# Kernel optimization log

Hardware: AMD Instinct MI355X
Metric: run time of the kernel (lower is better)

The kernel has to match this reference:

```python
import jax, jax.numpy as jnp
import numpy as np

TOP_K = 2


def setup_inputs() -> dict:
    key = jax.random.key(0)
    ks = jax.random.split(key, 7)
    B, T, C, E = 4, 2048, 1024, 8
    H = 4 * C
    s = 0.02
    return {
        "x": jax.random.normal(ks[0], (B, T, C), dtype=jnp.float32),
        "w_gate": jax.random.normal(ks[1], (C, E), dtype=jnp.float32) * s,
        "w1": jax.random.normal(ks[2], (E, C, H), dtype=jnp.float32) * s,
        "b1": jnp.zeros((E, H), dtype=jnp.float32),
        "w2": jax.random.normal(ks[3], (E, H, C), dtype=jnp.float32) * s,
        "b2": jnp.zeros((E, C), dtype=jnp.float32),
    }


def reference(x, w_gate, w1, b1, w2, b2):
    # Eval-mode MoE: noiseless gating (self.training=False), dropout inactive.
    B, T, C = x.shape
    E = w1.shape[0]
    xf = x.reshape(-1, C)                                # [N, C]
    logits = xf @ w_gate                                 # [N, E] clean logits
    top_vals, top_idx = jax.lax.top_k(logits, TOP_K)     # [N, K]
    scores = jax.nn.softmax(top_vals, axis=-1)           # [N, K]
    out = jnp.zeros_like(xf)
    for e in range(E):                                   # fixed small expert loop
        # combine weight per token for expert e (0 if not routed -> same math
        # as the original masked gather/scatter, since 0*expert_out == 0)
        w = jnp.sum(scores * (top_idx == e), axis=-1)    # [N]
        h = jax.nn.gelu(xf @ w1[e] + b1[e], approximate=False)  # [N, 4C]
        y = h @ w2[e] + b2[e]                            # [N, C]
        out = out + w[:, None] * y
    return out.reshape(B, T, C)
```

## Files before the change

kernel.cpp:

```cpp
#include <hip/hip_runtime.h>

#define NTOK 8192
#define CDIM 1024
#define ENUM 8
#define HDIM 4096

typedef unsigned short u16;
typedef unsigned int u32;
typedef __attribute__((ext_vector_type(8))) short s16x8;
typedef __attribute__((ext_vector_type(4))) float f32x4;
typedef __attribute__((ext_vector_type(4))) u32 u32x4;
typedef __attribute__((ext_vector_type(2))) u32 u32x2;

static __device__ __forceinline__ u16 f2bf(float f) {
  union { float f; u32 u; } v; v.f = f;
  u32 r = v.u + 0x7fffu + ((v.u >> 16) & 1u);
  return (u16)(r >> 16);
}
static __device__ __forceinline__ u32 pack2(float a, float b) {
  return (u32)f2bf(a) | ((u32)f2bf(b) << 16);
}
static __device__ __forceinline__ float bflo(u32 v) {
  union { u32 u; float f; } x; x.u = v << 16; return x.f;
}
static __device__ __forceinline__ float bfhi(u32 v) {
  union { u32 u; float f; } x; x.u = v & 0xffff0000u; return x.f;
}

typedef __attribute__((address_space(1))) const void gvoid;
typedef __attribute__((address_space(3))) void lvoid;
static __device__ __forceinline__ void gload16(const u16* g, u16* l) {
  __builtin_amdgcn_global_load_lds((gvoid*)g, (lvoid*)l, 16, 0, 0);
}

static __device__ __forceinline__ float gelu_fast(float v) {
  float u = v * (1.5957691216f + 0.1426929792f * v * v);
  return v / (1.f + __expf(-u));
}

__global__ void wconv_kernel(const float* __restrict__ w, u16* __restrict__ wt,
                             int K, int N) {
  __shared__ float lt[64][65];
  const int e = blockIdx.z, k0 = blockIdx.y * 64, n0 = blockIdx.x * 64;
  const float* src = w + (size_t)e * K * N;
  u16* dst = wt + (size_t)e * N * K;
  const int t = threadIdx.x;
  const int tr = t >> 4, tc = (t & 15) * 4;
#pragma unroll
  for (int i = 0; i < 4; ++i) {
    f32x4 v = __builtin_nontemporal_load(
        (const f32x4*)(src + (size_t)(k0 + tr + i * 16) * N + n0 + tc));
    lt[tr + i * 16][tc] = v.x; lt[tr + i * 16][tc + 1] = v.y;
    lt[tr + i * 16][tc + 2] = v.z; lt[tr + i * 16][tc + 3] = v.w;
  }
  __syncthreads();
#pragma unroll
  for (int i = 0; i < 4; ++i) {
    int n = tr + i * 16;
    uint2 o;
    o.x = pack2(lt[tc + 0][n], lt[tc + 1][n]);
    o.y = pack2(lt[tc + 2][n], lt[tc + 3][n]);
    *(uint2*)(dst + (size_t)(n0 + n) * K + k0 + tc) = o;
  }
}

__global__ void gate_kernel(const float* __restrict__ x, const float* __restrict__ wg,
                            int* __restrict__ cnt, int* __restrict__ tok_e,
                            float* __restrict__ tok_w) {
  __shared__ int lcnt[ENUM];
  const int tid = threadIdx.x;
  if (tid < ENUM) lcnt[tid] = 0;
  __syncthreads();
  const int wv = tid >> 6, lane = tid & 63;
  const int tbase = blockIdx.x * 32 + wv * 8;
  for (int t = 0; t < 8; ++t) {
    const int gw = tbase + t;
    const float* xr = x + (size_t)gw * CDIM;
    float acc[ENUM];
#pragma unroll
    for (int e = 0; e < ENUM; ++e) acc[e] = 0.f;
#pragma unroll 4
    for (int i = 0; i < CDIM / 64; ++i) {
      int c = i * 64 + lane;
      float xv = xr[c];
      float4 wa = *(const float4*)(wg + (size_t)c * ENUM);
      float4 wb = *(const float4*)(wg + (size_t)c * ENUM + 4);
      acc[0] += xv * wa.x; acc[1] += xv * wa.y; acc[2] += xv * wa.z; acc[3] += xv * wa.w;
      acc[4] += xv * wb.x; acc[5] += xv * wb.y; acc[6] += xv * wb.z; acc[7] += xv * wb.w;
    }
#pragma unroll
    for (int e = 0; e < ENUM; ++e) {
#pragma unroll
      for (int off = 32; off > 0; off >>= 1) acc[e] += __shfl_xor(acc[e], off);
    }
    if (lane == 0) {
      int i0 = 0; float v0 = acc[0];
#pragma unroll
      for (int e = 1; e < ENUM; ++e) if (acc[e] > v0) { v0 = acc[e]; i0 = e; }
      int i1 = -1; float v1 = -3.4e38f;
#pragma unroll
      for (int e = 0; e < ENUM; ++e) if (e != i0 && acc[e] > v1) { v1 = acc[e]; i1 = e; }
      float ex = expf(v1 - v0);
      float den = 1.f + ex;
      tok_e[gw * 2] = i0;     tok_w[gw * 2] = 1.f / den;
      tok_e[gw * 2 + 1] = i1; tok_w[gw * 2 + 1] = ex / den;
      atomicAdd(&lcnt[i0], 1); atomicAdd(&lcnt[i1], 1);
    }
  }
  __syncthreads();
  if (tid < ENUM) {
    int v = lcnt[tid];
    if (v) atomicAdd(&cnt[tid], v);
  }
}

__global__ void offsets_kernel(const int* __restrict__ cnt, int* __restrict__ offs) {
  if (threadIdx.x == 0 && blockIdx.x == 0) {
    int s = 0;
    for (int e = 0; e < ENUM; ++e) { offs[e] = s; s += cnt[e]; }
  }
}

__global__ void assign_kernel(const int* __restrict__ tok_e, const int* __restrict__ offs,
                              int* __restrict__ fill, int* __restrict__ slot_tok,
                              int* __restrict__ tok_slot) {
  __shared__ int lfill[ENUM], lbase[ENUM];
  const int tid = threadIdx.x;
  if (tid < ENUM) lfill[tid] = 0;
  __syncthreads();
  const int n = blockIdx.x * 256 + tid;
  const int e0 = tok_e[n * 2], e1 = tok_e[n * 2 + 1];
  const int p0 = atomicAdd(&lfill[e0], 1);
  const int p1 = atomicAdd(&lfill[e1], 1);
  __syncthreads();
  if (tid < ENUM) lbase[tid] = lfill[tid] ? atomicAdd(&fill[tid], lfill[tid]) : 0;
  __syncthreads();
  const int s0 = offs[e0] + lbase[e0] + p0;
  const int s1 = offs[e1] + lbase[e1] + p1;
  slot_tok[s0] = n; tok_slot[n * 2] = s0;
  slot_tok[s1] = n; tok_slot[n * 2 + 1] = s1;
}

__global__ void gather_kernel(const float* __restrict__ x, const int* __restrict__ slot_tok,
                              u16* __restrict__ xg) {
  int gid = blockIdx.x * blockDim.x + threadIdx.x;
  int slot = gid >> 8;
  int c4 = (gid & 255) * 4;
  int tok = slot_tok[slot];
  float4 v = *(const float4*)(x + (size_t)tok * CDIM + c4);
  uint2 o; o.x = pack2(v.x, v.y); o.y = pack2(v.z, v.w);
  *(uint2*)(xg + (size_t)slot * CDIM + c4) = o;
}

template <int PHASE>
__global__ __launch_bounds__(256, 2) void moe_gemm(
    const u16* __restrict__ Ag, const u16* __restrict__ Bt, const float* __restrict__ bias,
    u16* __restrict__ outp,
    const int* __restrict__ cnts, const int* __restrict__ offs,
    int K, int Nn) {
  const int e = blockIdx.z;
  const int cnt = cnts[e];
  const int NT = gridDim.x;
  const int MTC = gridDim.y >> 3;
  const int r = blockIdx.y * NT + blockIdx.x;
  const int k = r & 7;
  const int i = r >> 3;
  const int ck = (k + e) & 7;
  const int mt = ck * MTC + (i % MTC);
  const int nt = i / MTC;
  if (mt * 128 >= cnt) return;
  const int moff = offs[e];
  const int tid = threadIdx.x;
  const int wv = tid >> 6, ln = tid & 63;
  const int lr = ln & 15, lg = ln >> 4;
  const int wm = wv >> 1, wn = wv & 1;

  __shared__ __align__(16) u16 lds[2][128 * 64];
  u16* lA = lds[0];
  u16* lB = lds[1];

  const u16* Abase = Ag + (size_t)moff * K;
  const u16* Bbase = Bt + (size_t)e * Nn * K + (size_t)nt * 128 * K;

  const int srow = ln >> 3;
  const int sk = (((ln & 7) ^ srow)) * 8;

  f32x4 acc[4][4];
#pragma unroll
  for (int m = 0; m < 4; ++m)
#pragma unroll
    for (int n = 0; n < 4; ++n) {
      acc[m][n][0] = 0.f; acc[m][n][1] = 0.f; acc[m][n][2] = 0.f; acc[m][n][3] = 0.f;
    }

  const int nk = K / 64;
  for (int kt = 0; kt < nk; ++kt) {
#pragma unroll
    for (int i4 = 0; i4 < 4; ++i4) {
      int c = wv * 4 + i4;
      int ra = mt * 128 + c * 8 + srow;
      ra = ra < cnt ? ra : cnt - 1;
      gload16(Abase + (size_t)ra * K + kt * 64 + sk, lA + c * 512);
      gload16(Bbase + (size_t)(c * 8 + srow) * K + kt * 64 + sk, lB + c * 512);
    }
    __syncthreads();
#pragma unroll
    for (int ko = 0; ko < 2; ++ko) {
      s16x8 af[4], bfr[4];
      const int lsw = lr & 7;
#pragma unroll
      for (int m = 0; m < 4; ++m)
        af[m] = *(const s16x8*)(lA + (wm * 64 + m * 16 + lr) * 64 + ((ko * 4 + lg) ^ lsw) * 8);
#pragma unroll
      for (int n = 0; n < 4; ++n)
        bfr[n] = *(const s16x8*)(lB + (wn * 64 + n * 16 + lr) * 64 + ((ko * 4 + lg) ^ lsw) * 8);
#pragma unroll
      for (int m = 0; m < 4; ++m)
#pragma unroll
        for (int n = 0; n < 4; ++n)
          acc[m][n] = __builtin_amdgcn_mfma_f32_16x16x32_bf16(af[m], bfr[n], acc[m][n], 0, 0, 0);
    }
    __syncthreads();
  }

  u16* lT = lds[0];
  float bv[4];
#pragma unroll
  for (int n = 0; n < 4; ++n) bv[n] = bias[(size_t)e * Nn + nt * 128 + wn * 64 + n * 16 + lr];
#pragma unroll
  for (int m = 0; m < 4; ++m) {
#pragma unroll
    for (int r4 = 0; r4 < 4; ++r4) {
      int row = wm * 64 + m * 16 + lg * 4 + r4;
#pragma unroll
      for (int n = 0; n < 4; ++n) {
        int col = wn * 64 + n * 16 + lr;
        float v = acc[m][n][r4] + bv[n];
        if (PHASE == 1) v = gelu_fast(v);
        lT[row * 128 + col] = f2bf(v);
      }
    }
  }
  __syncthreads();
#pragma unroll
  for (int j = 0; j < 8; ++j) {
    int u = j * 256 + tid;
    int row = u >> 4;
    int colb = (u & 15) * 8;
    int grow = mt * 128 + row;
    if (grow < cnt) {
      u32x4 v = ((const u32x4*)lT)[u];
      *(u32x4*)(outp + (size_t)(moff + grow) * Nn + nt * 128 + colb) = v;
    }
  }
}

__global__ void combine_kernel(const u16* __restrict__ y, const int* __restrict__ tok_slot,
                               const float* __restrict__ tok_w, float* __restrict__ out) {
  int gid = blockIdx.x * blockDim.x + threadIdx.x;
  int n = gid >> 8;
  int c4 = (gid & 255) * 4;
  int s0 = tok_slot[n * 2], s1 = tok_slot[n * 2 + 1];
  float w0 = tok_w[n * 2], w1 = tok_w[n * 2 + 1];
  u32x2 a = __builtin_nontemporal_load((const u32x2*)(y + (size_t)s0 * CDIM + c4));
  u32x2 b = __builtin_nontemporal_load((const u32x2*)(y + (size_t)s1 * CDIM + c4));
  float4 o;
  o.x = w0 * bflo(a.x) + w1 * bflo(b.x);
  o.y = w0 * bfhi(a.x) + w1 * bfhi(b.x);
  o.z = w0 * bflo(a.y) + w1 * bflo(b.y);
  o.w = w0 * bfhi(a.y) + w1 * bfhi(b.y);
  *(float4*)(out + (size_t)n * CDIM + c4) = o;
}

extern "C" void kernel_launch(void* const* d_in, const int* in_sizes, int n_in,
                              void* d_out, int out_size, void* d_ws, size_t ws_size,
                              hipStream_t stream) {
  const float* x  = (const float*)d_in[0];
  const float* wg = (const float*)d_in[1];
  const float* w1 = (const float*)d_in[2];
  const float* b1 = (const float*)d_in[3];
  const float* w2 = (const float*)d_in[4];
  const float* b2 = (const float*)d_in[5];
  float* out = (float*)d_out;

  char* ws = (char*)d_ws;
  int* cnt  = (int*)ws;
  int* fill = cnt + 8;
  int* offs = cnt + 16;
  size_t off = 256;
  int*   tok_e    = (int*)(ws + off);   off += (size_t)NTOK * 2 * 4;
  float* tok_w    = (float*)(ws + off); off += (size_t)NTOK * 2 * 4;
  int*   slot_tok = (int*)(ws + off);   off += (size_t)NTOK * 2 * 4;
  int*   tok_slot = (int*)(ws + off);   off += (size_t)NTOK * 2 * 4;
  u16*   xg  = (u16*)(ws + off); off += (size_t)NTOK * 2 * CDIM * 2;
  u16*   h   = (u16*)(ws + off); off += (size_t)NTOK * 2 * HDIM * 2;
  u16*   y   = (u16*)(ws + off); off += (size_t)NTOK * 2 * CDIM * 2;
  u16*   w1t = (u16*)(ws + off); off += (size_t)ENUM * CDIM * HDIM * 2;
  u16*   w2t = (u16*)(ws + off); off += (size_t)ENUM * HDIM * CDIM * 2;

  hipMemsetAsync(cnt, 0, 64, stream);

  wconv_kernel<<<dim3(HDIM / 64, CDIM / 64, ENUM), 256, 0, stream>>>(w1, w1t, CDIM, HDIM);
  wconv_kernel<<<dim3(CDIM / 64, HDIM / 64, ENUM), 256, 0, stream>>>(w2, w2t, HDIM, CDIM);

  gate_kernel<<<NTOK / 32, 256, 0, stream>>>(x, wg, cnt, tok_e, tok_w);
  offsets_kernel<<<1, 64, 0, stream>>>(cnt, offs);
  assign_kernel<<<NTOK / 256, 256, 0, stream>>>(tok_e, offs, fill, slot_tok, tok_slot);
  gather_kernel<<<NTOK * 2, 256, 0, stream>>>(x, slot_tok, xg);

  moe_gemm<1><<<dim3(HDIM / 128, NTOK / 128, ENUM), 256, 0, stream>>>(
      xg, w1t, b1, h, cnt, offs, CDIM, HDIM);
  moe_gemm<2><<<dim3(CDIM / 128, NTOK / 128, ENUM), 256, 0, stream>>>(
      h, w2t, b2, y, cnt, offs, HDIM, CDIM);

  combine_kernel<<<NTOK, 256, 0, stream>>>(y, tok_slot, tok_w, out);
}
```

Before: 507.7 us.

## Convert grouped MoE GEMM to persistent kernel with XCD-aware tile striding

Replaces the 3D grid (most of whose blocks exit early because of empty expert tiles) with a fixed 1024-block persistent launch. Each block strides over the flattened (expert, m-tile, n-tile) space and skips empty tiles, with m-tiles mapped by XCD index to keep B-weight tiles local to each chiplet's L2. This aims to remove launch and dispatch overhead for the many early-exiting blocks and to improve cache locality. It adds a loop-carried barrier per tile and drops the occupancy hint from launch bounds, which risks load imbalance across blocks and changes register allocation.

```diff
diff --git a/kernel.cpp b/kernel.cpp
--- a/kernel.cpp
+++ b/kernel.cpp
@@ -152,106 +152,108 @@
   *(uint2*)(xg + (size_t)slot * CDIM + c4) = o;
 }
 
-template <int PHASE>
-__global__ __launch_bounds__(256, 2) void moe_gemm(
+template <int PHASE, int NT>
+__global__ __launch_bounds__(256) void moe_gemm(
     const u16* __restrict__ Ag, const u16* __restrict__ Bt, const float* __restrict__ bias,
     u16* __restrict__ outp,
     const int* __restrict__ cnts, const int* __restrict__ offs,
     int K, int Nn) {
-  const int e = blockIdx.z;
-  const int cnt = cnts[e];
-  const int NT = gridDim.x;
-  const int MTC = gridDim.y >> 3;
-  const int r = blockIdx.y * NT + blockIdx.x;
-  const int k = r & 7;
-  const int i = r >> 3;
-  const int ck = (k + e) & 7;
-  const int mt = ck * MTC + (i % MTC);
-  const int nt = i / MTC;
-  if (mt * 128 >= cnt) return;
-  const int moff = offs[e];
+  const int xcd = blockIdx.x & 7;
+  const int wkr = blockIdx.x >> 3;
   const int tid = threadIdx.x;
   const int wv = tid >> 6, ln = tid & 63;
   const int lr = ln & 15, lg = ln >> 4;
   const int wm = wv >> 1, wn = wv & 1;
+  const int srow = ln >> 3;
+  const int sk = (((ln & 7) ^ srow)) * 8;
 
   __shared__ __align__(16) u16 lds[2][128 * 64];
   u16* lA = lds[0];
   u16* lB = lds[1];
 
-  const u16* Abase = Ag + (size_t)moff * K;
-  const u16* Bbase = Bt + (size_t)e * Nn * K + (size_t)nt * 128 * K;
-
-  const int srow = ln >> 3;
-  const int sk = (((ln & 7) ^ srow)) * 8;
-
-  f32x4 acc[4][4];
-#pragma unroll
-  for (int m = 0; m < 4; ++m)
-#pragma unroll
-    for (int n = 0; n < 4; ++n) {
-      acc[m][n][0] = 0.f; acc[m][n][1] = 0.f; acc[m][n][2] = 0.f; acc[m][n][3] = 0.f;
-    }
-
-  const int nk = K / 64;
-  for (int kt = 0; kt < nk; ++kt) {
-#pragma unroll
-    for (int i4 = 0; i4 < 4; ++i4) {
-      int c = wv * 4 + i4;
-      int ra = mt * 128 + c * 8 + srow;
-      ra = ra < cnt ? ra : cnt - 1;
-      gload16(Abase + (size_t)ra * K + kt * 64 + sk, lA + c * 512);
-      gload16(Bbase + (size_t)(c * 8 + srow) * K + kt * 64 + sk, lB + c * 512);
+  const int TILES = 64 * NT;
+  for (int v = wkr; v < TILES; v += 128) {
+    const int e = v / (8 * NT);
+    const int rem = v % (8 * NT);
+    const int mt = (((xcd + e) & 7) << 3) + rem / NT;
+    const int nt = rem % NT;
+    const int cnt = cnts[e];
+    if (mt * 128 >= cnt) continue;
+    const int moff = offs[e];
+
+    const u16* Abase = Ag + (size_t)moff * K;
+    const u16* Bbase = Bt + (size_t)e * Nn * K + (size_t)nt * 128 * K;
+
+    f32x4 acc[4][4];
+#pragma unroll
+    for (int m = 0; m < 4; ++m)
+#pragma unroll
+      for (int n = 0; n < 4; ++n) {
+        acc[m][n][0] = 0.f; acc[m][n][1] = 0.f; acc[m][n][2] = 0.f; acc[m][n][3] = 0.f;
+      }
+
+    const int nk = K / 64;
+    for (int kt = 0; kt < nk; ++kt) {
+#pragma unroll
+      for (int i4 = 0; i4 < 4; ++i4) {
+        int c = wv * 4 + i4;
+        int ra = mt * 128 + c * 8 + srow;
+        ra = ra < cnt ? ra : cnt - 1;
+        gload16(Abase + (size_t)ra * K + kt * 64 + sk, lA + c * 512);
+        gload16(Bbase + (size_t)(c * 8 + srow) * K + kt * 64 + sk, lB + c * 512);
+      }
+      __syncthreads();
+#pragma unroll
+      for (int ko = 0; ko < 2; ++ko) {
+        s16x8 af[4], bfr[4];
+        const int lsw = lr & 7;
+#pragma unroll
+        for (int m = 0; m < 4; ++m)
+          af[m] = *(const s16x8*)(lA + (wm * 64 + m * 16 + lr) * 64 + ((ko * 4 + lg) ^ lsw) * 8);
+#pragma unroll
+        for (int n = 0; n < 4; ++n)
+          bfr[n] = *(const s16x8*)(lB + (wn * 64 + n * 16 + lr) * 64 + ((ko * 4 + lg) ^ lsw) * 8);
+#pragma unroll
+        for (int m = 0; m < 4; ++m)
+#pragma unroll
+          for (int n = 0; n < 4; ++n)
+            acc[m][n] = __builtin_amdgcn_mfma_f32_16x16x32_bf16(af[m], bfr[n], acc[m][n], 0, 0, 0);
+      }
+      __syncthreads();
+    }
+
+    u16* lT = lds[0];
+    float bv[4];
+#pragma unroll
+    for (int n = 0; n < 4; ++n)
+      bv[n] = bias[(size_t)e * Nn + nt * 128 + wn * 64 + n * 16 + lr];
+#pragma unroll
+    for (int m = 0; m < 4; ++m) {
+#pragma unroll
+      for (int r4 = 0; r4 < 4; ++r4) {
+        int row = wm * 64 + m * 16 + lg * 4 + r4;
+#pragma unroll
+        for (int n = 0; n < 4; ++n) {
+          int col = wn * 64 + n * 16 + lr;
+          float val = acc[m][n][r4] + bv[n];
+          if (PHASE == 1) val = gelu_fast(val);
+          lT[row * 128 + col] = f2bf(val);
+        }
+      }
     }
     __syncthreads();
 #pragma unroll
-    for (int ko = 0; ko < 2; ++ko) {
-      s16x8 af[4], bfr[4];
-      const int lsw = lr & 7;
-#pragma unroll
-      for (int m = 0; m < 4; ++m)
-        af[m] = *(const s16x8*)(lA + (wm * 64 + m * 16 + lr) * 64 + ((ko * 4 + lg) ^ lsw) * 8);
-#pragma unroll
-      for (int n = 0; n < 4; ++n)
-        bfr[n] = *(const s16x8*)(lB + (wn * 64 + n * 16 + lr) * 64 + ((ko * 4 + lg) ^ lsw) * 8);
-#pragma unroll
-      for (int m = 0; m < 4; ++m)
-#pragma unroll
-        for (int n = 0; n < 4; ++n)
-          acc[m][n] = __builtin_amdgcn_mfma_f32_16x16x32_bf16(af[m], bfr[n], acc[m][n], 0, 0, 0);
+    for (int j = 0; j < 8; ++j) {
+      int u = j * 256 + tid;
+      int row = u >> 4;
+      int colb = (u & 15) * 8;
+      int grow = mt * 128 + row;
+      if (grow < cnt) {
+        u32x4 vv = ((const u32x4*)lT)[u];
+        *(u32x4*)(outp + (size_t)(moff + grow) * Nn + nt * 128 + colb) = vv;
+      }
     }
     __syncthreads();
-  }
-
-  u16* lT = lds[0];
-  float bv[4];
-#pragma unroll
-  for (int n = 0; n < 4; ++n) bv[n] = bias[(size_t)e * Nn + nt * 128 + wn * 64 + n * 16 + lr];
-#pragma unroll
-  for (int m = 0; m < 4; ++m) {
-#pragma unroll
-    for (int r4 = 0; r4 < 4; ++r4) {
-      int row = wm * 64 + m * 16 + lg * 4 + r4;
-#pragma unroll
-      for (int n = 0; n < 4; ++n) {
-        int col = wn * 64 + n * 16 + lr;
-        float v = acc[m][n][r4] + bv[n];
-        if (PHASE == 1) v = gelu_fast(v);
-        lT[row * 128 + col] = f2bf(v);
-      }
-    }
-  }
-  __syncthreads();
-#pragma unroll
-  for (int j = 0; j < 8; ++j) {
-    int u = j * 256 + tid;
-    int row = u >> 4;
-    int colb = (u & 15) * 8;
-    int grow = mt * 128 + row;
-    if (grow < cnt) {
-      u32x4 v = ((const u32x4*)lT)[u];
-      *(u32x4*)(outp + (size_t)(moff + grow) * Nn + nt * 128 + colb) = v;
-    }
   }
 }
 
@@ -308,9 +310,9 @@
   assign_kernel<<<NTOK / 256, 256, 0, stream>>>(tok_e, offs, fill, slot_tok, tok_slot);
   gather_kernel<<<NTOK * 2, 256, 0, stream>>>(x, slot_tok, xg);
 
-  moe_gemm<1><<<dim3(HDIM / 128, NTOK / 128, ENUM), 256, 0, stream>>>(
+  moe_gemm<1, HDIM / 128><<<1024, 256, 0, stream>>>(
       xg, w1t, b1, h, cnt, offs, CDIM, HDIM);
-  moe_gemm<2><<<dim3(CDIM / 128, NTOK / 128, ENUM), 256, 0, stream>>>(
+  moe_gemm<2, CDIM / 128><<<1024, 256, 0, stream>>>(
       h, w2t, b2, y, cnt, offs, HDIM, CDIM);
 
   combine_kernel<<<NTOK, 256, 0, stream>>>(y, tok_slot, tok_w, out);
```

After: 643.8 us. 1.27x slower.

## Double-buffer LDS tiles to overlap global loads with MFMA compute

Applied to the files above, without the earlier changes.

Doubles the shared-memory tile buffers so the next K-slice of A and B is prefetched into the alternate buffer while MFMAs run on the current one. The loop drops from two barriers per iteration to one. Per-thread row offsets, including the clamp on the A row, are hoisted out of the K loop. This doubles LDS use to 64KB per block, which may reduce occupancy. Correctness also depends on how gload16 waits on the async global-to-LDS copy before the single barrier.

```diff
diff --git a/kernel.cpp b/kernel.cpp
--- a/kernel.cpp
+++ b/kernel.cpp
@@ -175,9 +175,7 @@
   const int lr = ln & 15, lg = ln >> 4;
   const int wm = wv >> 1, wn = wv & 1;
 
-  __shared__ __align__(16) u16 lds[2][128 * 64];
-  u16* lA = lds[0];
-  u16* lB = lds[1];
+  __shared__ __align__(16) u16 lds[2][2][8192];
 
   const u16* Abase = Ag + (size_t)moff * K;
   const u16* Bbase = Bt + (size_t)e * Nn * K + (size_t)nt * 128 * K;
@@ -185,6 +183,16 @@
   const int srow = ln >> 3;
   const int sk = (((ln & 7) ^ srow)) * 8;
 
+  size_t ao[4], bo[4];
+#pragma unroll
+  for (int c4 = 0; c4 < 4; ++c4) {
+    int c = wv * 4 + c4;
+    int ra = mt * 128 + c * 8 + srow;
+    ra = ra < cnt ? ra : cnt - 1;
+    ao[c4] = (size_t)ra * K + sk;
+    bo[c4] = (size_t)(c * 8 + srow) * K + sk;
+  }
+
   f32x4 acc[4][4];
 #pragma unroll
   for (int m = 0; m < 4; ++m)
@@ -194,16 +202,29 @@
     }
 
   const int nk = K / 64;
+
+#pragma unroll
+  for (int c4 = 0; c4 < 4; ++c4) {
+    int c = wv * 4 + c4;
+    gload16(Abase + ao[c4], &lds[0][0][0] + c * 512);
+    gload16(Bbase + bo[c4], &lds[0][1][0] + c * 512);
+  }
+  __syncthreads();
+
+  int cur = 0;
   for (int kt = 0; kt < nk; ++kt) {
-#pragma unroll
-    for (int i4 = 0; i4 < 4; ++i4) {
-      int c = wv * 4 + i4;
-      int ra = mt * 128 + c * 8 + srow;
-      ra = ra < cnt ? ra : cnt - 1;
-      gload16(Abase + (size_t)ra * K + kt * 64 + sk, lA + c * 512);
-      gload16(Bbase + (size_t)(c * 8 + srow) * K + kt * 64 + sk, lB + c * 512);
-    }
-    __syncthreads();
+    if (kt + 1 < nk) {
+      const int kadd = (kt + 1) * 64;
+      const int nxt = cur ^ 1;
+#pragma unroll
+      for (int c4 = 0; c4 < 4; ++c4) {
+        int c = wv * 4 + c4;
+        gload16(Abase + ao[c4] + kadd, &lds[nxt][0][0] + c * 512);
+        gload16(Bbase + bo[c4] + kadd, &lds[nxt][1][0] + c * 512);
+      }
+    }
+    const u16* lA = &lds[cur][0][0];
+    const u16* lB = &lds[cur][1][0];
 #pragma unroll
     for (int ko = 0; ko < 2; ++ko) {
       s16x8 af[4], bfr[4];
@@ -221,9 +242,10 @@
           acc[m][n] = __builtin_amdgcn_mfma_f32_16x16x32_bf16(af[m], bfr[n], acc[m][n], 0, 0, 0);
     }
     __syncthreads();
-  }
-
-  u16* lT = lds[0];
+    cur ^= 1;
+  }
+
+  u16* lT = &lds[0][0][0];
   float bv[4];
 #pragma unroll
   for (int n = 0; n < 4; ++n) bv[n] = bias[(size_t)e * Nn + nt * 128 + wn * 64 + n * 16 + lr];
```

New measurement: 552.2 us. 8.8% more time.

## Enlarge MoE GEMM tile to 256x128 with 512-thread blocks

Applied to the files above, without the earlier changes.

The expert GEMM block tile grows from 128x128 to 256x128 rows, using 8 waves (512 threads) so the B (weight) tile loaded into LDS is reused across twice as many token rows. Global load offsets are precomputed once outside the K loop. The epilogue writes output in two 128-row halves through the shared LDS staging buffer, with extra barriers. The change cuts weight traffic per output, but it raises LDS use to 48KB and launch_bounds(512,4) may force register spilling with the 64 accumulators per thread.

```diff
diff --git a/kernel.cpp b/kernel.cpp
--- a/kernel.cpp
+++ b/kernel.cpp
@@ -153,7 +153,7 @@
 }
 
 template <int PHASE>
-__global__ __launch_bounds__(256, 2) void moe_gemm(
+__global__ __launch_bounds__(512, 4) void moe_gemm(
     const u16* __restrict__ Ag, const u16* __restrict__ Bt, const float* __restrict__ bias,
     u16* __restrict__ outp,
     const int* __restrict__ cnts, const int* __restrict__ offs,
@@ -168,16 +168,16 @@
   const int ck = (k + e) & 7;
   const int mt = ck * MTC + (i % MTC);
   const int nt = i / MTC;
-  if (mt * 128 >= cnt) return;
+  if (mt * 256 >= cnt) return;
   const int moff = offs[e];
   const int tid = threadIdx.x;
   const int wv = tid >> 6, ln = tid & 63;
   const int lr = ln & 15, lg = ln >> 4;
   const int wm = wv >> 1, wn = wv & 1;
 
-  __shared__ __align__(16) u16 lds[2][128 * 64];
-  u16* lA = lds[0];
-  u16* lB = lds[1];
+  __shared__ __align__(16) u16 lds[24576];
+  u16* lA = lds;
+  u16* lB = lds + 16384;
 
   const u16* Abase = Ag + (size_t)moff * K;
   const u16* Bbase = Bt + (size_t)e * Nn * K + (size_t)nt * 128 * K;
@@ -185,6 +185,20 @@
   const int srow = ln >> 3;
   const int sk = (((ln & 7) ^ srow)) * 8;
 
+  size_t ao[4], bo[2];
+#pragma unroll
+  for (int c4 = 0; c4 < 4; ++c4) {
+    int c = wv * 4 + c4;
+    int ra = mt * 256 + c * 8 + srow;
+    ra = ra < cnt ? ra : cnt - 1;
+    ao[c4] = (size_t)ra * K + sk;
+  }
+#pragma unroll
+  for (int c2 = 0; c2 < 2; ++c2) {
+    int c = wv * 2 + c2;
+    bo[c2] = (size_t)(c * 8 + srow) * K + sk;
+  }
+
   f32x4 acc[4][4];
 #pragma unroll
   for (int m = 0; m < 4; ++m)
@@ -195,14 +209,13 @@
 
   const int nk = K / 64;
   for (int kt = 0; kt < nk; ++kt) {
-#pragma unroll
-    for (int i4 = 0; i4 < 4; ++i4) {
-      int c = wv * 4 + i4;
-      int ra = mt * 128 + c * 8 + srow;
-      ra = ra < cnt ? ra : cnt - 1;
-      gload16(Abase + (size_t)ra * K + kt * 64 + sk, lA + c * 512);
-      gload16(Bbase + (size_t)(c * 8 + srow) * K + kt * 64 + sk, lB + c * 512);
-    }
+    const int kadd = kt * 64;
+#pragma unroll
+    for (int c4 = 0; c4 < 4; ++c4)
+      gload16(Abase + ao[c4] + kadd, lA + (wv * 4 + c4) * 512);
+#pragma unroll
+    for (int c2 = 0; c2 < 2; ++c2)
+      gload16(Bbase + bo[c2] + kadd, lB + (wv * 2 + c2) * 512);
     __syncthreads();
 #pragma unroll
     for (int ko = 0; ko < 2; ++ko) {
@@ -223,35 +236,42 @@
     __syncthreads();
   }
 
-  u16* lT = lds[0];
+  u16* lT = lds;
   float bv[4];
 #pragma unroll
   for (int n = 0; n < 4; ++n) bv[n] = bias[(size_t)e * Nn + nt * 128 + wn * 64 + n * 16 + lr];
 #pragma unroll
-  for (int m = 0; m < 4; ++m) {
-#pragma unroll
-    for (int r4 = 0; r4 < 4; ++r4) {
-      int row = wm * 64 + m * 16 + lg * 4 + r4;
-#pragma unroll
-      for (int n = 0; n < 4; ++n) {
-        int col = wn * 64 + n * 16 + lr;
-        float v = acc[m][n][r4] + bv[n];
-        if (PHASE == 1) v = gelu_fast(v);
-        lT[row * 128 + col] = f2bf(v);
+  for (int h = 0; h < 2; ++h) {
+    if ((wm >> 1) == h) {
+      const int rbase = (wm & 1) * 64;
+#pragma unroll
+      for (int m = 0; m < 4; ++m) {
+#pragma unroll
+        for (int r4 = 0; r4 < 4; ++r4) {
+          int row = rbase + m * 16 + lg * 4 + r4;
+#pragma unroll
+          for (int n = 0; n < 4; ++n) {
+            int col = wn * 64 + n * 16 + lr;
+            float v = acc[m][n][r4] + bv[n];
+            if (PHASE == 1) v = gelu_fast(v);
+            lT[row * 128 + col] = f2bf(v);
+          }
+        }
       }
     }
-  }
-  __syncthreads();
-#pragma unroll
-  for (int j = 0; j < 8; ++j) {
-    int u = j * 256 + tid;
-    int row = u >> 4;
-    int colb = (u & 15) * 8;
-    int grow = mt * 128 + row;
-    if (grow < cnt) {
-      u32x4 v = ((const u32x4*)lT)[u];
-      *(u32x4*)(outp + (size_t)(moff + grow) * Nn + nt * 128 + colb) = v;
-    }
+    __syncthreads();
+#pragma unroll
+    for (int j = 0; j < 4; ++j) {
+      int u = j * 512 + tid;
+      int row = u >> 4;
+      int colb = (u & 15) * 8;
+      int grow = mt * 256 + h * 128 + row;
+      if (grow < cnt) {
+        u32x4 v = ((const u32x4*)lT)[u];
+        *(u32x4*)(outp + (size_t)(moff + grow) * Nn + nt * 128 + colb) = v;
+      }
+    }
+    __syncthreads();
   }
 }
 
@@ -308,9 +328,9 @@
   assign_kernel<<<NTOK / 256, 256, 0, stream>>>(tok_e, offs, fill, slot_tok, tok_slot);
   gather_kernel<<<NTOK * 2, 256, 0, stream>>>(x, slot_tok, xg);
 
-  moe_gemm<1><<<dim3(HDIM / 128, NTOK / 128, ENUM), 256, 0, stream>>>(
+  moe_gemm<1><<<dim3(HDIM / 128, NTOK / 256, ENUM), 512, 0, stream>>>(
       xg, w1t, b1, h, cnt, offs, CDIM, HDIM);
-  moe_gemm<2><<<dim3(CDIM / 128, NTOK / 128, ENUM), 256, 0, stream>>>(
+  moe_gemm<2><<<dim3(CDIM / 128, NTOK / 256, ENUM), 512, 0, stream>>>(
       h, w2t, b2, y, cnt, offs, HDIM, CDIM);
 
   combine_kernel<<<NTOK, 256, 0, stream>>>(y, tok_slot, tok_w, out);
```

Measured after the change: 571.0 us. +12.4%, slower.
